# Kernel tuning notes

Hardware: AMD Instinct MI355X
Metric: run time of the kernel (lower is better)

The kernel has to match this reference:

```python
import jax, jax.numpy as jnp
import numpy as np

N = 100000
E = 800000
IN_DIM = 128
H = 4
D = 32
HD = H * D  # 128
EPS = 1e-5
NEG_SLOPE = 0.2


def setup_inputs() -> dict:
    key = jax.random.key(0)
    ks = jax.random.split(key, 12)
    feat = jax.random.normal(ks[0], (N, IN_DIM), dtype=jnp.float32)
    src = jax.random.randint(ks[1], (E,), 0, N)
    dst = jax.random.randint(ks[2], (E,), 0, N)
    s = 1.0 / np.sqrt(IN_DIM)
    W_src = jax.random.uniform(ks[3], (HD, IN_DIM), jnp.float32, -s, s)
    b_src = jax.random.uniform(ks[4], (HD,), jnp.float32, -s, s)
    attn_l = jax.random.normal(ks[5], (1, H, D), dtype=jnp.float32) * np.sqrt(2.0 / (H * D + 1)) * np.sqrt(2.0)
    attn_r = jax.random.normal(ks[6], (1, H, D), dtype=jnp.float32) * np.sqrt(2.0 / (H * D + 1)) * np.sqrt(2.0)
    W_skip = jax.random.uniform(ks[7], (HD, IN_DIM), jnp.float32, -s, s)
    b_skip = jax.random.uniform(ks[8], (HD,), jnp.float32, -s, s)
    sg = 1.0 / np.sqrt(3 * HD)
    W_gate = jax.random.uniform(ks[9], (1, 3 * HD), jnp.float32, -sg, sg)
    b_gate = jax.random.uniform(ks[10], (1,), jnp.float32, -sg, sg)
    ln_g = jnp.ones((HD,), jnp.float32)
    ln_b = jnp.zeros((HD,), jnp.float32)
    prelu_a = jnp.full((1,), 0.25, jnp.float32)
    return {"feat": feat, "src": src, "dst": dst, "W_src": W_src, "b_src": b_src,
            "attn_l": attn_l, "attn_r": attn_r, "W_skip": W_skip, "b_skip": b_skip,
            "W_gate": W_gate, "b_gate": b_gate, "ln_g": ln_g, "ln_b": ln_b,
            "prelu_a": prelu_a}


def reference(feat, src, dst, W_src, b_src, attn_l, attn_r, W_skip, b_skip,
              W_gate, b_gate, ln_g, ln_b, prelu_a):
    # node projection -> [N, H, D]
    feat_src = (feat @ W_src.T + b_src).reshape(N, H, D)
    el = jnp.sum(feat_src * attn_l, axis=-1)  # [N, H]
    er = jnp.sum(feat_src * attn_r, axis=-1)  # [N, H]
    # per-edge logits with leaky relu
    e = el[src] + er[dst]                      # [E, H]
    e = jnp.where(e >= 0, e, NEG_SLOPE * e)
    # edge softmax over incoming edges of each dst node
    emax = jax.ops.segment_max(e, dst, num_segments=N)   # [N, H]
    ex = jnp.exp(e - emax[dst])                          # [E, H]
    esum = jax.ops.segment_sum(ex, dst, num_segments=N)  # [N, H]
    a = ex / esum[dst]                                   # [E, H]
    # weighted aggregation: sum_e a_e * ft[src_e]
    m = feat_src[src] * a[:, :, None]                    # [E, H, D]
    rst = jax.ops.segment_sum(m, dst, num_segments=N).reshape(N, HD)
    # gated skip connection
    skip = feat @ W_skip.T + b_skip                      # [N, HD]
    g_in = jnp.concatenate([rst, skip, rst - skip], axis=-1)
    gate = jax.nn.sigmoid(g_in @ W_gate.T + b_gate)      # [N, 1]
    rst = gate * rst + (1.0 - gate) * skip
    # layer norm
    mu = jnp.mean(rst, axis=-1, keepdims=True)
    var = jnp.var(rst, axis=-1, keepdims=True)
    y = (rst - mu) / jnp.sqrt(var + EPS) * ln_g + ln_b
    # PReLU (single shared alpha)
    return jnp.where(y >= 0, y, prelu_a[0] * y)
```

## Files before the change

kernel.cpp:

```cpp
#include <hip/hip_runtime.h>

typedef __attribute__((ext_vector_type(8))) short short8;
typedef __attribute__((ext_vector_type(4))) float v4f;

__device__ __forceinline__ ushort f2bf(float x) {
    unsigned u = __float_as_uint(x);
    u = u + 0x7fffu + ((u >> 16) & 1u);
    return (ushort)(u >> 16);
}
__device__ __forceinline__ float bflo(unsigned u) { return __uint_as_float(u << 16); }
__device__ __forceinline__ float bfhi(unsigned u) { return __uint_as_float(u & 0xffff0000u); }

#define CPAD 16
#define SLOT 32
#define GGRID 512
#define CHSZ 4096

__global__ __launch_bounds__(256) void k_edges(
    const int* __restrict__ src, const int* __restrict__ dst,
    int* __restrict__ counts_p, int* __restrict__ padcsr,
    int E_, int ns8, int n)
{
    const int slice = blockIdx.x & 7;
    const int chunk = blockIdx.x >> 3;
    const int lo = slice * ns8;
    int hi = lo + ns8; if (hi > n) hi = n;
    const unsigned span = (unsigned)(hi - lo);

    int cend = (chunk + 1) * CHSZ; if (cend > E_) cend = E_;
    for (int off = chunk * CHSZ + threadIdx.x * 4; off < cend; off += 1024) {
        if (off + 4 <= cend) {
            int4 d4 = *(const int4*)(dst + off);
            int4 s4 = *(const int4*)(src + off);
            if ((unsigned)(d4.x - lo) < span) {
                int r = atomicAdd(&counts_p[(size_t)d4.x * CPAD], 1);
                if (r < SLOT) padcsr[(size_t)d4.x * SLOT + r] = s4.x;
            }
            if ((unsigned)(d4.y - lo) < span) {
                int r = atomicAdd(&counts_p[(size_t)d4.y * CPAD], 1);
                if (r < SLOT) padcsr[(size_t)d4.y * SLOT + r] = s4.y;
            }
            if ((unsigned)(d4.z - lo) < span) {
                int r = atomicAdd(&counts_p[(size_t)d4.z * CPAD], 1);
                if (r < SLOT) padcsr[(size_t)d4.z * SLOT + r] = s4.z;
            }
            if ((unsigned)(d4.w - lo) < span) {
                int r = atomicAdd(&counts_p[(size_t)d4.w * CPAD], 1);
                if (r < SLOT) padcsr[(size_t)d4.w * SLOT + r] = s4.w;
            }
        } else {
            for (int q = off; q < cend; ++q) {
                int d = dst[q];
                if ((unsigned)(d - lo) < span) {
                    int r = atomicAdd(&counts_p[(size_t)d * CPAD], 1);
                    if (r < SLOT) padcsr[(size_t)d * SLOT + r] = src[q];
                }
            }
        }
    }
}

__global__ __launch_bounds__(256, 2) void k_gemm(
    const float* __restrict__ feat, const float* __restrict__ Wsrc,
    const float* __restrict__ Wskip,
    const float* __restrict__ bsrc, const float* __restrict__ bskip,
    const float* __restrict__ attn_l, const float* __restrict__ attn_r,
    ushort* __restrict__ feat_src, ushort* __restrict__ skip_bf,
    float* __restrict__ el, float* __restrict__ er, int n)
{
    __shared__ float sA[16384];
    const int tid = threadIdx.x;
    const int wave = tid >> 6, lane = tid & 63;
    const int quad = lane >> 4, l16 = lane & 15;
    const int n0 = wave * 64;
    const int ntile = (n + 63) >> 6;

    short8 bb[4][4];
    #pragma unroll
    for (int nt = 0; nt < 4; ++nt) {
        int r = n0 + l16 + nt * 16;
        const float* wr = (r < 128) ? (Wsrc + (size_t)r * 128)
                                    : (Wskip + (size_t)(r - 128) * 128);
        #pragma unroll
        for (int k = 0; k < 4; ++k) {
            float4 w0 = *(const float4*)(wr + quad * 8 + k * 32);
            float4 w1 = *(const float4*)(wr + quad * 8 + k * 32 + 4);
            short8 v;
            v[0] = (short)f2bf(w0.x); v[1] = (short)f2bf(w0.y);
            v[2] = (short)f2bf(w0.z); v[3] = (short)f2bf(w0.w);
            v[4] = (short)f2bf(w1.x); v[5] = (short)f2bf(w1.y);
            v[6] = (short)f2bf(w1.z); v[7] = (short)f2bf(w1.w);
            bb[nt][k] = v;
            asm volatile("" : "+v"(bb[nt][k]));
        }
    }

    float4 bias[4], al[4], ar[4];
    #pragma unroll
    for (int nt = 0; nt < 4; ++nt) {
        int cb = n0 + nt * 16 + quad * 4;
        bias[nt] = (n0 < 128) ? *(const float4*)(bsrc + cb)
                              : *(const float4*)(bskip + (cb - 128));
        al[nt] = *(const float4*)(attn_l + (cb & 127));
        ar[nt] = *(const float4*)(attn_r + (cb & 127));
    }

    const int trow = tid >> 5;
    const int scb  = ((tid & 31) * 16) ^ ((trow & 7) << 4);
    const char* gbase = (const char*)feat;

    auto stage = [&](int tt, int buf) {
        #pragma unroll
        for (int i = 0; i < 8; ++i) {
            int grow = tt * 64 + i * 8 + trow;
            if (grow > n - 1) grow = n - 1;
            const void* g = gbase + (size_t)grow * 512 + scb;
            float* lp = sA + buf * 8192 + i * 1024 + wave * 256;
            __builtin_amdgcn_global_load_lds(
                (const __attribute__((address_space(1))) void*)g,
                (__attribute__((address_space(3))) void*)lp, 16, 0, 0);
        }
    };

    int t = blockIdx.x;
    if (t >= ntile) return;
    stage(t, 0);
    int p = 0;
    bool first = true;

    for (; t < ntile; t += GGRID) {
        int tn = t + GGRID;
        bool pre = (tn < ntile);
        if (pre) stage(tn, p ^ 1);
        if (!pre)       asm volatile("s_waitcnt vmcnt(0)" ::: "memory");
        else if (first) asm volatile("s_waitcnt vmcnt(8)" ::: "memory");
        else            asm volatile("s_waitcnt vmcnt(24)" ::: "memory");
        first = false;
        __builtin_amdgcn_s_barrier();
        __builtin_amdgcn_sched_barrier(0);

        #pragma unroll
        for (int s = 0; s < 2; ++s) {
            const int row0 = t * 64 + s * 32;
            v4f acc[2][4] = {};
            const char* sAB = (const char*)sA + p * 32768 + s * 16384;
            const int sw = (l16 & 7) << 4;
            #pragma unroll
            for (int k = 0; k < 4; ++k) {
                int c = quad * 32 + k * 128;
                float4 f0 = *(const float4*)(sAB + l16 * 512 + ((c     ) ^ sw));
                float4 f1 = *(const float4*)(sAB + l16 * 512 + ((c + 16) ^ sw));
                float4 g0 = *(const float4*)(sAB + (l16 + 16) * 512 + ((c     ) ^ sw));
                float4 g1 = *(const float4*)(sAB + (l16 + 16) * 512 + ((c + 16) ^ sw));
                short8 a0, a1;
                a0[0] = (short)f2bf(f0.x); a0[1] = (short)f2bf(f0.y);
                a0[2] = (short)f2bf(f0.z); a0[3] = (short)f2bf(f0.w);
                a0[4] = (short)f2bf(f1.x); a0[5] = (short)f2bf(f1.y);
                a0[6] = (short)f2bf(f1.z); a0[7] = (short)f2bf(f1.w);
                a1[0] = (short)f2bf(g0.x); a1[1] = (short)f2bf(g0.y);
                a1[2] = (short)f2bf(g0.z); a1[3] = (short)f2bf(g0.w);
                a1[4] = (short)f2bf(g1.x); a1[5] = (short)f2bf(g1.y);
                a1[6] = (short)f2bf(g1.z); a1[7] = (short)f2bf(g1.w);
                #pragma unroll
                for (int nt = 0; nt < 4; ++nt) {
                    acc[0][nt] = __builtin_amdgcn_mfma_f32_16x16x32_bf16(
                        bb[nt][k], a0, acc[0][nt], 0, 0, 0);
                    acc[1][nt] = __builtin_amdgcn_mfma_f32_16x16x32_bf16(
                        bb[nt][k], a1, acc[1][nt], 0, 0, 0);
                }
            }

            #pragma unroll
            for (int nt = 0; nt < 4; ++nt) {
                #pragma unroll
                for (int mt = 0; mt < 2; ++mt) {
                    acc[mt][nt][0] += bias[nt].x;
                    acc[mt][nt][1] += bias[nt].y;
                    acc[mt][nt][2] += bias[nt].z;
                    acc[mt][nt][3] += bias[nt].w;
                }
            }

            #pragma unroll
            for (int mt = 0; mt < 2; ++mt) {
                int row = row0 + mt * 16 + l16;
                if (row < n) {
                    #pragma unroll
                    for (int nt = 0; nt < 4; ++nt) {
                        int cb = n0 + nt * 16 + quad * 4;
                        unsigned lo = (unsigned)f2bf(acc[mt][nt][0]) |
                                      ((unsigned)f2bf(acc[mt][nt][1]) << 16);
                        unsigned hi = (unsigned)f2bf(acc[mt][nt][2]) |
                                      ((unsigned)f2bf(acc[mt][nt][3]) << 16);
                        uint2 pv = make_uint2(lo, hi);
                        if (n0 < 128) *(uint2*)(feat_src + (size_t)row * 128 + cb) = pv;
                        else          *(uint2*)(skip_bf  + (size_t)row * 128 + (cb - 128)) = pv;
                    }
                }
            }

            if (wave < 2) {
                const int hb = n0 >> 5;
                #pragma unroll
                for (int mt = 0; mt < 2; ++mt) {
                    float pl0 = 0.f, pl1 = 0.f, pr0 = 0.f, pr1 = 0.f;
                    #pragma unroll
                    for (int i = 0; i < 4; ++i) {
                        float a0v = acc[mt][0][i], a1v = acc[mt][1][i];
                        float a2v = acc[mt][2][i], a3v = acc[mt][3][i];
                        const float* pal0 = (const float*)&al[0]; const float* pal1 = (const float*)&al[1];
                        const float* pal2 = (const float*)&al[2]; const float* pal3 = (const float*)&al[3];
                        const float* par0 = (const float*)&ar[0]; const float* par1 = (const float*)&ar[1];
                        const float* par2 = (const float*)&ar[2]; const float* par3 = (const float*)&ar[3];
                        pl0 = fmaf(a0v, pal0[i], fmaf(a1v, pal1[i], pl0));
                        pl1 = fmaf(a2v, pal2[i], fmaf(a3v, pal3[i], pl1));
                        pr0 = fmaf(a0v, par0[i], fmaf(a1v, par1[i], pr0));
                        pr1 = fmaf(a2v, par2[i], fmaf(a3v, par3[i], pr1));
                    }
                    pl0 += __shfl_xor(pl0, 16); pl0 += __shfl_xor(pl0, 32);
                    pl1 += __shfl_xor(pl1, 16); pl1 += __shfl_xor(pl1, 32);
                    pr0 += __shfl_xor(pr0, 16); pr0 += __shfl_xor(pr0, 32);
                    pr1 += __shfl_xor(pr1, 16); pr1 += __shfl_xor(pr1, 32);
                    int row = row0 + mt * 16 + l16;
                    if (lane < 16 && row < n) {
                        *(float2*)(el + (size_t)row * 4 + hb) = make_float2(pl0, pl1);
                        *(float2*)(er + (size_t)row * 4 + hb) = make_float2(pr0, pr1);
                    }
                }
            }
        }

        __builtin_amdgcn_s_barrier();
        p ^= 1;
    }
}

__global__ __launch_bounds__(256) void k3_fused(
    const int* __restrict__ counts_p, const int* __restrict__ padcsr,
    const float* __restrict__ el, const float* __restrict__ er,
    const ushort* __restrict__ feat_src, const ushort* __restrict__ skip_bf,
    const float* __restrict__ Wg, const float* __restrict__ bg,
    const float* __restrict__ lng, const float* __restrict__ lnb,
    const float* __restrict__ pa, float* __restrict__ out, int n)
{
    int node = blockIdx.x * 8 + (threadIdx.x >> 5);
    if (node >= n) return;
    int l32 = threadIdx.x & 31;
    int j = l32 * 4;
    int h = l32 >> 3;

    int cnt = counts_p[(size_t)node * CPAD];
    if (cnt > SLOT) cnt = SLOT;
    int beg = node * SLOT, end = beg + cnt;
    float er_h = er[(size_t)node * 4 + h];
    const ushort* fbase = feat_src + j;

    float ac0 = 0.f, ac1 = 0.f, ac2 = 0.f, ac3 = 0.f;
    float bc0 = 0.f, bc1 = 0.f, bc2 = 0.f, bc3 = 0.f;
    float wsA = 0.f, wsB = 0.f;

    for (int p0 = beg; p0 < end; p0 += 32) {
        int pv = p0 + l32;
        int sv = padcsr[pv < end ? pv : end - 1];
        int cb = end - p0; if (cb > 32) cb = 32;
        for (int i = 0; i < cb; i += 4) {
            int s0 = __shfl(sv, i, 32),     s1 = __shfl(sv, i + 1, 32);
            int s2 = __shfl(sv, i + 2, 32), s3 = __shfl(sv, i + 3, 32);
            float e0 = el[(size_t)s0 * 4 + h], e1 = el[(size_t)s1 * 4 + h];
            float e2 = el[(size_t)s2 * 4 + h], e3 = el[(size_t)s3 * 4 + h];
            uint2 u0 = *(const uint2*)(fbase + (size_t)s0 * 128);
            uint2 u1 = *(const uint2*)(fbase + (size_t)s1 * 128);
            uint2 u2 = *(const uint2*)(fbase + (size_t)s2 * 128);
            uint2 u3 = *(const uint2*)(fbase + (size_t)s3 * 128);
            float t0 = e0 + er_h, t1 = e1 + er_h, t2 = e2 + er_h, t3 = e3 + er_h;
            float w0 = __expf(fmaxf(t0, 0.2f * t0));
            float w1 = (i + 1 < cb) ? __expf(fmaxf(t1, 0.2f * t1)) : 0.f;
            float w2 = (i + 2 < cb) ? __expf(fmaxf(t2, 0.2f * t2)) : 0.f;
            float w3 = (i + 3 < cb) ? __expf(fmaxf(t3, 0.2f * t3)) : 0.f;
            wsA += w0 + w2; wsB += w1 + w3;
            ac0 = fmaf(w0, bflo(u0.x), fmaf(w2, bflo(u2.x), ac0));
            ac1 = fmaf(w0, bfhi(u0.x), fmaf(w2, bfhi(u2.x), ac1));
            ac2 = fmaf(w0, bflo(u0.y), fmaf(w2, bflo(u2.y), ac2));
            ac3 = fmaf(w0, bfhi(u0.y), fmaf(w2, bfhi(u2.y), ac3));
            bc0 = fmaf(w1, bflo(u1.x), fmaf(w3, bflo(u3.x), bc0));
            bc1 = fmaf(w1, bfhi(u1.x), fmaf(w3, bfhi(u3.x), bc1));
            bc2 = fmaf(w1, bflo(u1.y), fmaf(w3, bflo(u3.y), bc2));
            bc3 = fmaf(w1, bfhi(u1.y), fmaf(w3, bfhi(u3.y), bc3));
        }
    }
    float wsum = wsA + wsB;
    float inv = (wsum > 0.f) ? 1.f / wsum : 0.f;
    float r0 = (ac0 + bc0) * inv, r1 = (ac1 + bc1) * inv;
    float r2 = (ac2 + bc2) * inv, r3 = (ac3 + bc3) * inv;

    uint2 su = *(const uint2*)(skip_bf + (size_t)node * 128 + j);
    float s0 = bflo(su.x), s1 = bfhi(su.x), s2 = bflo(su.y), s3 = bfhi(su.y);

    float4 wg0 = *(const float4*)(Wg + j);
    float4 wg1 = *(const float4*)(Wg + 128 + j);
    float4 wg2 = *(const float4*)(Wg + 256 + j);
    float g = r0 * wg0.x + s0 * wg1.x + (r0 - s0) * wg2.x
            + r1 * wg0.y + s1 * wg1.y + (r1 - s1) * wg2.y
            + r2 * wg0.z + s2 * wg1.z + (r2 - s2) * wg2.z
            + r3 * wg0.w + s3 * wg1.w + (r3 - s3) * wg2.w;
    #pragma unroll
    for (int m = 1; m < 32; m <<= 1) g += __shfl_xor(g, m, 32);
    float gate = 1.f / (1.f + __expf(-(g + bg[0])));

    float x0 = gate * r0 + (1.f - gate) * s0;
    float x1 = gate * r1 + (1.f - gate) * s1;
    float x2 = gate * r2 + (1.f - gate) * s2;
    float x3 = gate * r3 + (1.f - gate) * s3;

    float sm = (x0 + x1) + (x2 + x3);
    float sq = (x0 * x0 + x1 * x1) + (x2 * x2 + x3 * x3);
    #pragma unroll
    for (int m = 1; m < 32; m <<= 1) {
        sm += __shfl_xor(sm, m, 32);
        sq += __shfl_xor(sq, m, 32);
    }
    float mu = sm * (1.f / 128.f);
    float var = sq * (1.f / 128.f) - mu * mu;
    float rs = rsqrtf(var + 1e-5f);
    float alpha = pa[0];
    float4 lg = *(const float4*)(lng + j);
    float4 lb = *(const float4*)(lnb + j);
    float y0 = (x0 - mu) * rs * lg.x + lb.x;
    float y1 = (x1 - mu) * rs * lg.y + lb.y;
    float y2 = (x2 - mu) * rs * lg.z + lb.z;
    float y3 = (x3 - mu) * rs * lg.w + lb.w;
    y0 = y0 >= 0.f ? y0 : alpha * y0;
    y1 = y1 >= 0.f ? y1 : alpha * y1;
    y2 = y2 >= 0.f ? y2 : alpha * y2;
    y3 = y3 >= 0.f ? y3 : alpha * y3;
    *(float4*)(out + (size_t)node * 128 + j) = make_float4(y0, y1, y2, y3);
}

extern "C" void kernel_launch(void* const* d_in, const int* in_sizes, int n_in,
                              void* d_out, int out_size, void* d_ws, size_t ws_size,
                              hipStream_t stream)
{
    const float* feat   = (const float*)d_in[0];
    const int*   src    = (const int*)d_in[1];
    const int*   dst    = (const int*)d_in[2];
    const float* Wsrc   = (const float*)d_in[3];
    const float* bsrc   = (const float*)d_in[4];
    const float* attn_l = (const float*)d_in[5];
    const float* attn_r = (const float*)d_in[6];
    const float* Wskip  = (const float*)d_in[7];
    const float* bskip  = (const float*)d_in[8];
    const float* Wg     = (const float*)d_in[9];
    const float* bg     = (const float*)d_in[10];
    const float* lng    = (const float*)d_in[11];
    const float* lnb    = (const float*)d_in[12];
    const float* pa     = (const float*)d_in[13];

    const int n = in_sizes[0] / 128;
    const int E = in_sizes[1];
    float* out = (float*)d_out;

    float*  el       = (float*)d_ws;
    float*  er       = el + (size_t)n * 4;
    ushort* feat_src = (ushort*)(er + (size_t)n * 4);
    ushort* skip_bf  = feat_src + (size_t)n * 128;
    int*    counts_p = (int*)(skip_bf + (size_t)n * 128);
    int*    padcsr   = counts_p + (size_t)n * CPAD;

    hipMemsetAsync(counts_p, 0, (size_t)n * CPAD * sizeof(int), stream);

    int ns8 = (n + 7) / 8;
    int nchunk = (E + CHSZ - 1) / CHSZ;
    k_edges<<<nchunk * 8, 256, 0, stream>>>(
        src, dst, counts_p, padcsr, E, ns8, n);

    k_gemm<<<GGRID, 256, 0, stream>>>(
        feat, Wsrc, Wskip, bsrc, bskip, attn_l, attn_r,
        feat_src, skip_bf, el, er, n);

    k3_fused<<<(n + 7) / 8, 256, 0, stream>>>(
        counts_p, padcsr, el, er, feat_src, skip_bf, Wg, bg, lng, lnb, pa, out, n);
}
```

Before: 234.2 us.

## Fold count zeroing into GEMM, shrink count padding, use 16 lanes per node

The separate memset of the per-node edge counters is replaced by extra blocks in the GEMM launch that zero the counters, and the edge-bucketing kernel now runs after the GEMM. The counter padding stride drops from 16 to 4 ints, so less memory is cleared and touched. The aggregation kernel now gives each node 16 lanes holding 8 features each, with 128-bit gathers, so each wave covers more nodes and issues fewer, wider loads. In exchange each lane holds more registers, and atomics on counters packed closer together may contend more.

```diff
diff --git a/kernel.cpp b/kernel.cpp
--- a/kernel.cpp
+++ b/kernel.cpp
@@ -11,54 +11,10 @@
 __device__ __forceinline__ float bflo(unsigned u) { return __uint_as_float(u << 16); }
 __device__ __forceinline__ float bfhi(unsigned u) { return __uint_as_float(u & 0xffff0000u); }
 
-#define CPAD 16
+#define CPAD 4
 #define SLOT 32
 #define GGRID 512
 #define CHSZ 4096
-
-__global__ __launch_bounds__(256) void k_edges(
-    const int* __restrict__ src, const int* __restrict__ dst,
-    int* __restrict__ counts_p, int* __restrict__ padcsr,
-    int E_, int ns8, int n)
-{
-    const int slice = blockIdx.x & 7;
-    const int chunk = blockIdx.x >> 3;
-    const int lo = slice * ns8;
-    int hi = lo + ns8; if (hi > n) hi = n;
-    const unsigned span = (unsigned)(hi - lo);
-
-    int cend = (chunk + 1) * CHSZ; if (cend > E_) cend = E_;
-    for (int off = chunk * CHSZ + threadIdx.x * 4; off < cend; off += 1024) {
-        if (off + 4 <= cend) {
-            int4 d4 = *(const int4*)(dst + off);
-            int4 s4 = *(const int4*)(src + off);
-            if ((unsigned)(d4.x - lo) < span) {
-                int r = atomicAdd(&counts_p[(size_t)d4.x * CPAD], 1);
-                if (r < SLOT) padcsr[(size_t)d4.x * SLOT + r] = s4.x;
-            }
-            if ((unsigned)(d4.y - lo) < span) {
-                int r = atomicAdd(&counts_p[(size_t)d4.y * CPAD], 1);
-                if (r < SLOT) padcsr[(size_t)d4.y * SLOT + r] = s4.y;
-            }
-            if ((unsigned)(d4.z - lo) < span) {
-                int r = atomicAdd(&counts_p[(size_t)d4.z * CPAD], 1);
-                if (r < SLOT) padcsr[(size_t)d4.z * SLOT + r] = s4.z;
-            }
-            if ((unsigned)(d4.w - lo) < span) {
-                int r = atomicAdd(&counts_p[(size_t)d4.w * CPAD], 1);
-                if (r < SLOT) padcsr[(size_t)d4.w * SLOT + r] = s4.w;
-            }
-        } else {
-            for (int q = off; q < cend; ++q) {
-                int d = dst[q];
-                if ((unsigned)(d - lo) < span) {
-                    int r = atomicAdd(&counts_p[(size_t)d * CPAD], 1);
-                    if (r < SLOT) padcsr[(size_t)d * SLOT + r] = src[q];
-                }
-            }
-        }
-    }
-}
 
 __global__ __launch_bounds__(256, 2) void k_gemm(
     const float* __restrict__ feat, const float* __restrict__ Wsrc,
@@ -66,10 +22,18 @@
     const float* __restrict__ bsrc, const float* __restrict__ bskip,
     const float* __restrict__ attn_l, const float* __restrict__ attn_r,
     ushort* __restrict__ feat_src, ushort* __restrict__ skip_bf,
-    float* __restrict__ el, float* __restrict__ er, int n)
+    float* __restrict__ el, float* __restrict__ er,
+    int* __restrict__ counts_p, int ncnt, int n)
 {
     __shared__ float sA[16384];
     const int tid = threadIdx.x;
+
+    if (blockIdx.x >= GGRID) {
+        int i = ((blockIdx.x - GGRID) * 256 + tid) * 4;
+        if (i < ncnt) *(int4*)(counts_p + i) = make_int4(0, 0, 0, 0);
+        return;
+    }
+
     const int wave = tid >> 6, lane = tid & 63;
     const int quad = lane >> 4, l16 = lane & 15;
     const int n0 = wave * 64;
@@ -235,6 +199,50 @@
     }
 }
 
+__global__ __launch_bounds__(256) void k_edges(
+    const int* __restrict__ src, const int* __restrict__ dst,
+    int* __restrict__ counts_p, int* __restrict__ padcsr,
+    int E_, int ns8, int n)
+{
+    const int slice = blockIdx.x & 7;
+    const int chunk = blockIdx.x >> 3;
+    const int lo = slice * ns8;
+    int hi = lo + ns8; if (hi > n) hi = n;
+    const unsigned span = (unsigned)(hi - lo);
+
+    int cend = (chunk + 1) * CHSZ; if (cend > E_) cend = E_;
+    for (int off = chunk * CHSZ + threadIdx.x * 4; off < cend; off += 1024) {
+        if (off + 4 <= cend) {
+            int4 d4 = *(const int4*)(dst + off);
+            int4 s4 = *(const int4*)(src + off);
+            if ((unsigned)(d4.x - lo) < span) {
+                int r = atomicAdd(&counts_p[(size_t)d4.x * CPAD], 1);
+                if (r < SLOT) padcsr[(size_t)d4.x * SLOT + r] = s4.x;
+            }
+            if ((unsigned)(d4.y - lo) < span) {
+                int r = atomicAdd(&counts_p[(size_t)d4.y * CPAD], 1);
+                if (r < SLOT) padcsr[(size_t)d4.y * SLOT + r] = s4.y;
+            }
+            if ((unsigned)(d4.z - lo) < span) {
+                int r = atomicAdd(&counts_p[(size_t)d4.z * CPAD], 1);
+                if (r < SLOT) padcsr[(size_t)d4.z * SLOT + r] = s4.z;
+            }
+            if ((unsigned)(d4.w - lo) < span) {
+                int r = atomicAdd(&counts_p[(size_t)d4.w * CPAD], 1);
+                if (r < SLOT) padcsr[(size_t)d4.w * SLOT + r] = s4.w;
+            }
+        } else {
+            for (int q = off; q < cend; ++q) {
+                int d = dst[q];
+                if ((unsigned)(d - lo) < span) {
+                    int r = atomicAdd(&counts_p[(size_t)d * CPAD], 1);
+                    if (r < SLOT) padcsr[(size_t)d * SLOT + r] = src[q];
+                }
+            }
+        }
+    }
+}
+
 __global__ __launch_bounds__(256) void k3_fused(
     const int* __restrict__ counts_p, const int* __restrict__ padcsr,
     const float* __restrict__ el, const float* __restrict__ er,
@@ -243,11 +251,11 @@
     const float* __restrict__ lng, const float* __restrict__ lnb,
     const float* __restrict__ pa, float* __restrict__ out, int n)
 {
-    int node = blockIdx.x * 8 + (threadIdx.x >> 5);
+    int node = blockIdx.x * 16 + (threadIdx.x >> 4);
     if (node >= n) return;
-    int l32 = threadIdx.x & 31;
-    int j = l32 * 4;
-    int h = l32 >> 3;
+    int l16 = threadIdx.x & 15;
+    int j = l16 * 8;
+    int h = l16 >> 2;
 
     int cnt = counts_p[(size_t)node * CPAD];
     if (cnt > SLOT) cnt = SLOT;
@@ -255,85 +263,120 @@
     float er_h = er[(size_t)node * 4 + h];
     const ushort* fbase = feat_src + j;
 
-    float ac0 = 0.f, ac1 = 0.f, ac2 = 0.f, ac3 = 0.f;
-    float bc0 = 0.f, bc1 = 0.f, bc2 = 0.f, bc3 = 0.f;
+    float aA0=0.f,aA1=0.f,aA2=0.f,aA3=0.f,aA4=0.f,aA5=0.f,aA6=0.f,aA7=0.f;
+    float aB0=0.f,aB1=0.f,aB2=0.f,aB3=0.f,aB4=0.f,aB5=0.f,aB6=0.f,aB7=0.f;
     float wsA = 0.f, wsB = 0.f;
 
-    for (int p0 = beg; p0 < end; p0 += 32) {
-        int pv = p0 + l32;
+    for (int p0 = beg; p0 < end; p0 += 16) {
+        int pv = p0 + l16;
         int sv = padcsr[pv < end ? pv : end - 1];
-        int cb = end - p0; if (cb > 32) cb = 32;
+        int cb = end - p0; if (cb > 16) cb = 16;
         for (int i = 0; i < cb; i += 4) {
-            int s0 = __shfl(sv, i, 32),     s1 = __shfl(sv, i + 1, 32);
-            int s2 = __shfl(sv, i + 2, 32), s3 = __shfl(sv, i + 3, 32);
+            int s0 = __shfl(sv, i, 16),     s1 = __shfl(sv, i + 1, 16);
+            int s2 = __shfl(sv, i + 2, 16), s3 = __shfl(sv, i + 3, 16);
             float e0 = el[(size_t)s0 * 4 + h], e1 = el[(size_t)s1 * 4 + h];
             float e2 = el[(size_t)s2 * 4 + h], e3 = el[(size_t)s3 * 4 + h];
-            uint2 u0 = *(const uint2*)(fbase + (size_t)s0 * 128);
-            uint2 u1 = *(const uint2*)(fbase + (size_t)s1 * 128);
-            uint2 u2 = *(const uint2*)(fbase + (size_t)s2 * 128);
-            uint2 u3 = *(const uint2*)(fbase + (size_t)s3 * 128);
+            uint4 u0 = *(const uint4*)(fbase + (size_t)s0 * 128);
+            uint4 u1 = *(const uint4*)(fbase + (size_t)s1 * 128);
+            uint4 u2 = *(const uint4*)(fbase + (size_t)s2 * 128);
+            uint4 u3 = *(const uint4*)(fbase + (size_t)s3 * 128);
             float t0 = e0 + er_h, t1 = e1 + er_h, t2 = e2 + er_h, t3 = e3 + er_h;
             float w0 = __expf(fmaxf(t0, 0.2f * t0));
             float w1 = (i + 1 < cb) ? __expf(fmaxf(t1, 0.2f * t1)) : 0.f;
             float w2 = (i + 2 < cb) ? __expf(fmaxf(t2, 0.2f * t2)) : 0.f;
             float w3 = (i + 3 < cb) ? __expf(fmaxf(t3, 0.2f * t3)) : 0.f;
             wsA += w0 + w2; wsB += w1 + w3;
-            ac0 = fmaf(w0, bflo(u0.x), fmaf(w2, bflo(u2.x), ac0));
-            ac1 = fmaf(w0, bfhi(u0.x), fmaf(w2, bfhi(u2.x), ac1));
-            ac2 = fmaf(w0, bflo(u0.y), fmaf(w2, bflo(u2.y), ac2));
-            ac3 = fmaf(w0, bfhi(u0.y), fmaf(w2, bfhi(u2.y), ac3));
-            bc0 = fmaf(w1, bflo(u1.x), fmaf(w3, bflo(u3.x), bc0));
-            bc1 = fmaf(w1, bfhi(u1.x), fmaf(w3, bfhi(u3.x), bc1));
-            bc2 = fmaf(w1, bflo(u1.y), fmaf(w3, bflo(u3.y), bc2));
-            bc3 = fmaf(w1, bfhi(u1.y), fmaf(w3, bfhi(u3.y), bc3));
+            aA0 = fmaf(w0, bflo(u0.x), fmaf(w2, bflo(u2.x), aA0));
+            aA1 = fmaf(w0, bfhi(u0.x), fmaf(w2, bfhi(u2.x), aA1));
+            aA2 = fmaf(w0, bflo(u0.y), fmaf(w2, bflo(u2.y), aA2));
+            aA3 = fmaf(w0, bfhi(u0.y), fmaf(w2, bfhi(u2.y), aA3));
+            aA4 = fmaf(w0, bflo(u0.z), fmaf(w2, bflo(u2.z), aA4));
+            aA5 = fmaf(w0, bfhi(u0.z), fmaf(w2, bfhi(u2.z), aA5));
+            aA6 = fmaf(w0, bflo(u0.w), fmaf(w2, bflo(u2.w), aA6));
+            aA7 = fmaf(w0, bfhi(u0.w), fmaf(w2, bfhi(u2.w), aA7));
+            aB0 = fmaf(w1, bflo(u1.x), fmaf(w3, bflo(u3.x), aB0));
+            aB1 = fmaf(w1, bfhi(u1.x), fmaf(w3, bfhi(u3.x), aB1));
+            aB2 = fmaf(w1, bflo(u1.y), fmaf(w3, bflo(u3.y), aB2));
+            aB3 = fmaf(w1, bfhi(u1.y), fmaf(w3, bfhi(u3.y), aB3));
+            aB4 = fmaf(w1, bflo(u1.z), fmaf(w3, bflo(u3.z), aB4));
+            aB5 = fmaf(w1, bfhi(u1.z), fmaf(w3, bfhi(u3.z), aB5));
+            aB6 = fmaf(w1, bflo(u1.w), fmaf(w3, bflo(u3.w), aB6));
+            aB7 = fmaf(w1, bfhi(u1.w), fmaf(w3, bfhi(u3.w), aB7));
         }
     }
     float wsum = wsA + wsB;
     float inv = (wsum > 0.f) ? 1.f / wsum : 0.f;
-    float r0 = (ac0 + bc0) * inv, r1 = (ac1 + bc1) * inv;
-    float r2 = (ac2 + bc2) * inv, r3 = (ac3 + bc3) * inv;
-
-    uint2 su = *(const uint2*)(skip_bf + (size_t)node * 128 + j);
+    float r0 = (aA0 + aB0) * inv, r1 = (aA1 + aB1) * inv;
+    float r2 = (aA2 + aB2) * inv, r3 = (aA3 + aB3) * inv;
+    float r4 = (aA4 + aB4) * inv, r5 = (aA5 + aB5) * inv;
+    float r6 = (aA6 + aB6) * inv, r7 = (aA7 + aB7) * inv;
+
+    uint4 su = *(const uint4*)(skip_bf + (size_t)node * 128 + j);
     float s0 = bflo(su.x), s1 = bfhi(su.x), s2 = bflo(su.y), s3 = bfhi(su.y);
-
-    float4 wg0 = *(const float4*)(Wg + j);
-    float4 wg1 = *(const float4*)(Wg + 128 + j);
-    float4 wg2 = *(const float4*)(Wg + 256 + j);
-    float g = r0 * wg0.x + s0 * wg1.x + (r0 - s0) * wg2.x
-            + r1 * wg0.y + s1 * wg1.y + (r1 - s1) * wg2.y
-            + r2 * wg0.z + s2 * wg1.z + (r2 - s2) * wg2.z
-            + r3 * wg0.w + s3 * wg1.w + (r3 - s3) * wg2.w;
+    float s4 = bflo(su.z), s5 = bfhi(su.z), s6 = bflo(su.w), s7 = bfhi(su.w);
+
+    float4 wgA0 = *(const float4*)(Wg + j);
+    float4 wgA1 = *(const float4*)(Wg + j + 4);
+    float4 wgB0 = *(const float4*)(Wg + 128 + j);
+    float4 wgB1 = *(const float4*)(Wg + 128 + j + 4);
+    float4 wgC0 = *(const float4*)(Wg + 256 + j);
+    float4 wgC1 = *(const float4*)(Wg + 256 + j + 4);
+    float g = r0 * wgA0.x + s0 * wgB0.x + (r0 - s0) * wgC0.x
+            + r1 * wgA0.y + s1 * wgB0.y + (r1 - s1) * wgC0.y
+            + r2 * wgA0.z + s2 * wgB0.z + (r2 - s2) * wgC0.z
+            + r3 * wgA0.w + s3 * wgB0.w + (r3 - s3) * wgC0.w
+            + r4 * wgA1.x + s4 * wgB1.x + (r4 - s4) * wgC1.x
+            + r5 * wgA1.y + s5 * wgB1.y + (r5 - s5) * wgC1.y
+            + r6 * wgA1.z + s6 * wgB1.z + (r6 - s6) * wgC1.z
+            + r7 * wgA1.w + s7 * wgB1.w + (r7 - s7) * wgC1.w;
     #pragma unroll
-    for (int m = 1; m < 32; m <<= 1) g += __shfl_xor(g, m, 32);
+    for (int m = 1; m < 16; m <<= 1) g += __shfl_xor(g, m, 16);
     float gate = 1.f / (1.f + __expf(-(g + bg[0])));
 
     float x0 = gate * r0 + (1.f - gate) * s0;
     float x1 = gate * r1 + (1.f - gate) * s1;
     float x2 = gate * r2 + (1.f - gate) * s2;
     float x3 = gate * r3 + (1.f - gate) * s3;
-
-    float sm = (x0 + x1) + (x2 + x3);
-    float sq = (x0 * x0 + x1 * x1) + (x2 * x2 + x3 * x3);
+    float x4 = gate * r4 + (1.f - gate) * s4;
+    float x5 = gate * r5 + (1.f - gate) * s5;
+    float x6 = gate * r6 + (1.f - gate) * s6;
+    float x7 = gate * r7 + (1.f - gate) * s7;
+
+    float sm = ((x0 + x1) + (x2 + x3)) + ((x4 + x5) + (x6 + x7));
+    float sq = ((x0 * x0 + x1 * x1) + (x2 * x2 + x3 * x3))
+             + ((x4 * x4 + x5 * x5) + (x6 * x6 + x7 * x7));
     #pragma unroll
-    for (int m = 1; m < 32; m <<= 1) {
-        sm += __shfl_xor(sm, m, 32);
-        sq += __shfl_xor(sq, m, 32);
+    for (int m = 1; m < 16; m <<= 1) {
+        sm += __shfl_xor(sm, m, 16);
+        sq += __shfl_xor(sq, m, 16);
     }
     float mu = sm * (1.f / 128.f);
     float var = sq * (1.f / 128.f) - mu * mu;
     float rs = rsqrtf(var + 1e-5f);
     float alpha = pa[0];
-    float4 lg = *(const float4*)(lng + j);
-    float4 lb = *(const float4*)(lnb + j);
-    float y0 = (x0 - mu) * rs * lg.x + lb.x;
-    float y1 = (x1 - mu) * rs * lg.y + lb.y;
-    float y2 = (x2 - mu) * rs * lg.z + lb.z;
-    float y3 = (x3 - mu) * rs * lg.w + lb.w;
+    float4 lg0 = *(const float4*)(lng + j);
+    float4 lg1 = *(const float4*)(lng + j + 4);
+    float4 lb0 = *(const float4*)(lnb + j);
+    float4 lb1 = *(const float4*)(lnb + j + 4);
+    float y0 = (x0 - mu) * rs * lg0.x + lb0.x;
+    float y1 = (x1 - mu) * rs * lg0.y + lb0.y;
+    float y2 = (x2 - mu) * rs * lg0.z + lb0.z;
+    float y3 = (x3 - mu) * rs * lg0.w + lb0.w;
+    float y4 = (x4 - mu) * rs * lg1.x + lb1.x;
+    float y5 = (x5 - mu) * rs * lg1.y + lb1.y;
+    float y6 = (x6 - mu) * rs * lg1.z + lb1.z;
+    float y7 = (x7 - mu) * rs * lg1.w + lb1.w;
     y0 = y0 >= 0.f ? y0 : alpha * y0;
     y1 = y1 >= 0.f ? y1 : alpha * y1;
     y2 = y2 >= 0.f ? y2 : alpha * y2;
     y3 = y3 >= 0.f ? y3 : alpha * y3;
-    *(float4*)(out + (size_t)node * 128 + j) = make_float4(y0, y1, y2, y3);
+    y4 = y4 >= 0.f ? y4 : alpha * y4;
+    y5 = y5 >= 0.f ? y5 : alpha * y5;
+    y6 = y6 >= 0.f ? y6 : alpha * y6;
+    y7 = y7 >= 0.f ? y7 : alpha * y7;
+    float* ob = out + (size_t)node * 128 + j;
+    *(float4*)(ob)     = make_float4(y0, y1, y2, y3);
+    *(float4*)(ob + 4) = make_float4(y4, y5, y6, y7);
 }
 
 extern "C" void kernel_launch(void* const* d_in, const int* in_sizes, int n_in,
@@ -366,17 +409,17 @@
     int*    counts_p = (int*)(skip_bf + (size_t)n * 128);
     int*    padcsr   = counts_p + (size_t)n * CPAD;
 
-    hipMemsetAsync(counts_p, 0, (size_t)n * CPAD * sizeof(int), stream);
+    int ncnt = n * CPAD;
+    int nzb = (ncnt + 1023) / 1024;
+    k_gemm<<<GGRID + nzb, 256, 0, stream>>>(
+        feat, Wsrc, Wskip, bsrc, bskip, attn_l, attn_r,
+        feat_src, skip_bf, el, er, counts_p, ncnt, n);
 
     int ns8 = (n + 7) / 8;
     int nchunk = (E + CHSZ - 1) / CHSZ;
     k_edges<<<nchunk * 8, 256, 0, stream>>>(
         src, dst, counts_p, padcsr, E, ns8, n);
 
-    k_gemm<<<GGRID, 256, 0, stream>>>(
-        feat, Wsrc, Wskip, bsrc, bskip, attn_l, attn_r,
-        feat_src, skip_bf, el, er, n);
-
-    k3_fused<<<(n + 7) / 8, 256, 0, stream>>>(
+    k3_fused<<<(n + 15) / 16, 256, 0, stream>>>(
         counts_p, padcsr, el, er, feat_src, skip_bf, Wg, bg, lng, lnb, pa, out, n);
 }
```

Result: faster. 228.9 us (-2.3%).
